# Optimization experiments

Measured on AMD Instinct MI355X. Metric: run time of the kernel, lower is better.

Reference implementation:

```python
import jax, jax.numpy as jnp
import numpy as np

N_NODES = 100000

def setup_inputs() -> dict:
    key = jax.random.key(0)
    k1, k2, k3, k4 = jax.random.split(key, 4)
    B, S, D, H = 50000, 10, 128, 128
    nodes = jax.random.randint(k1, (B,), 0, N_NODES, dtype=jnp.int64 if jax.config.jax_enable_x64 else jnp.int32)
    neigh_idx = jax.random.randint(k2, (B, S), 0, N_NODES, dtype=nodes.dtype)
    feature = jax.random.normal(k3, (N_NODES, D), dtype=jnp.float32)
    weight = jax.random.normal(k4, (2 * D, H), dtype=jnp.float32) * (1.0 / np.sqrt(2 * D))
    return {"nodes": nodes, "neigh_idx": neigh_idx, "feature": feature, "weight": weight}

def reference(nodes, neigh_idx, feature, weight):
    # Mean aggregation over sampled neighbors: [B, S, D] -> [B, D]
    neigh_feats = jnp.mean(feature[neigh_idx], axis=1)
    # Self features: [B, D]
    self_feats = feature[nodes]
    # Concat + linear + ReLU (gcn=False branch)
    combined = jnp.concatenate([self_feats, neigh_feats], axis=1)  # [B, 2D]
    return jax.nn.relu(combined @ weight)  # [B, H]
```

## Files before the change

### kernel.cpp

```cpp
#include <hip/hip_runtime.h>


typedef __attribute__((ext_vector_type(8))) short bf16x8;
typedef __attribute__((ext_vector_type(4))) float f32x4;

#define THREADS 512
#define B_TILE 64

__device__ __forceinline__ unsigned short f2bf(float x) {
  unsigned int u = __float_as_uint(x);
  u += 0x7fffu + ((u >> 16) & 1u);
  return (unsigned short)(u >> 16);
}

__global__ __launch_bounds__(THREADS, 1)
void sage_fused(const int* __restrict__ nodes,
                const int* __restrict__ neigh,
                const float* __restrict__ feat,
                const float* __restrict__ W,
                float* __restrict__ out,
                int B)
{
  constexpr int D = 128, K = 256, H = 128, S = 10;
  constexpr int STR = K + 8;

  __shared__ unsigned short Clds[B_TILE * STR];
  __shared__ unsigned short Wt[H * STR];

  const int t = threadIdx.x;
  const int block0 = blockIdx.x * B_TILE;

  {
    const float4* W4 = (const float4*)W;
#pragma unroll
    for (int i = 0; i < (K * H / 4) / THREADS; ++i) {
      int f4i = i * THREADS + t;
      float4 v = W4[f4i];
      int flat = f4i << 2;
      int k = flat >> 7;
      int h = flat & (H - 1);
      Wt[(h + 0) * STR + k] = f2bf(v.x);
      Wt[(h + 1) * STR + k] = f2bf(v.y);
      Wt[(h + 2) * STR + k] = f2bf(v.z);
      Wt[(h + 3) * STR + k] = f2bf(v.w);
    }
  }

  {
    const int r   = t >> 3;
    const int sub = t & 7;
    const int b   = block0 + r;
    ushort4* cself = (ushort4*)&Clds[r * STR];
    ushort4* cmean = (ushort4*)&Clds[r * STR + D];
    if (b < B) {
      const float4* fbase = (const float4*)feat;
      const long srow = (long)nodes[b] * (D / 4);
      float4 sf[4];
#pragma unroll
      for (int j = 0; j < 4; ++j) sf[j] = fbase[srow + j * 8 + sub];
      float ax[4], ay[4], az[4], aw[4];
#pragma unroll
      for (int j = 0; j < 4; ++j) { ax[j] = 0.f; ay[j] = 0.f; az[j] = 0.f; aw[j] = 0.f; }
#pragma unroll
      for (int s = 0; s < S; ++s) {
        const long nrow = (long)neigh[b * S + s] * (D / 4);
#pragma unroll
        for (int j = 0; j < 4; ++j) {
          float4 v = fbase[nrow + j * 8 + sub];
          ax[j] += v.x; ay[j] += v.y; az[j] += v.z; aw[j] += v.w;
        }
      }
#pragma unroll
      for (int j = 0; j < 4; ++j) {
        int q = j * 8 + sub;
        ushort4 sv, mv;
        sv.x = f2bf(sf[j].x); sv.y = f2bf(sf[j].y);
        sv.z = f2bf(sf[j].z); sv.w = f2bf(sf[j].w);
        mv.x = f2bf(ax[j] * 0.1f); mv.y = f2bf(ay[j] * 0.1f);
        mv.z = f2bf(az[j] * 0.1f); mv.w = f2bf(aw[j] * 0.1f);
        cself[q] = sv;
        cmean[q] = mv;
      }
    } else {
      ushort4 z; z.x = z.y = z.z = z.w = 0;
#pragma unroll
      for (int j = 0; j < 4; ++j) {
        int q = j * 8 + sub;
        cself[q] = z;
        cmean[q] = z;
      }
    }
  }
  __syncthreads();

  const int lane = t & 63;
  const int wave = t >> 6;
  const int m    = lane & 15;
  const int quad = lane >> 4;
  const int rbase = (wave & 1) * 32;
  const int cbase = (wave >> 1) * 32;

  f32x4 acc00 = {0.f, 0.f, 0.f, 0.f};
  f32x4 acc01 = {0.f, 0.f, 0.f, 0.f};
  f32x4 acc10 = {0.f, 0.f, 0.f, 0.f};
  f32x4 acc11 = {0.f, 0.f, 0.f, 0.f};

#pragma unroll
  for (int ks = 0; ks < K / 32; ++ks) {
    const int koff = ks * 32 + quad * 8;
    bf16x8 a0 = *(const bf16x8*)&Clds[(rbase      + m) * STR + koff];
    bf16x8 a1 = *(const bf16x8*)&Clds[(rbase + 16 + m) * STR + koff];
    bf16x8 b0 = *(const bf16x8*)&Wt[(cbase      + m) * STR + koff];
    bf16x8 b1 = *(const bf16x8*)&Wt[(cbase + 16 + m) * STR + koff];
    acc00 = __builtin_amdgcn_mfma_f32_16x16x32_bf16(a0, b0, acc00, 0, 0, 0);
    acc01 = __builtin_amdgcn_mfma_f32_16x16x32_bf16(a0, b1, acc01, 0, 0, 0);
    acc10 = __builtin_amdgcn_mfma_f32_16x16x32_bf16(a1, b0, acc10, 0, 0, 0);
    acc11 = __builtin_amdgcn_mfma_f32_16x16x32_bf16(a1, b1, acc11, 0, 0, 0);
  }

#pragma unroll
  for (int reg = 0; reg < 4; ++reg) {
    const int row0 = rbase + quad * 4 + reg;
    const int row1 = rbase + 16 + quad * 4 + reg;
    const int gb0 = block0 + row0;
    const int gb1 = block0 + row1;
    if (gb0 < B) {
      out[(size_t)gb0 * H + cbase      + m] = fmaxf(acc00[reg], 0.0f);
      out[(size_t)gb0 * H + cbase + 16 + m] = fmaxf(acc01[reg], 0.0f);
    }
    if (gb1 < B) {
      out[(size_t)gb1 * H + cbase      + m] = fmaxf(acc10[reg], 0.0f);
      out[(size_t)gb1 * H + cbase + 16 + m] = fmaxf(acc11[reg], 0.0f);
    }
  }
}

extern "C" void kernel_launch(void* const* d_in, const int* in_sizes, int n_in,
                              void* d_out, int out_size, void* d_ws, size_t ws_size,
                              hipStream_t stream) {
  const int*   nodes = (const int*)d_in[0];
  const int*   neigh = (const int*)d_in[1];
  const float* feat  = (const float*)d_in[2];
  const float* W     = (const float*)d_in[3];
  float*       out   = (float*)d_out;
  const int B = in_sizes[0];
  const int grid = (B + B_TILE - 1) / B_TILE;
  sage_fused<<<grid, THREADS, 0, stream>>>(nodes, neigh, feat, W, out, B);
}
```

Baseline: 149.7 us.

## Split fused SAGE kernel into weight-prep, gather and GEMM kernels

Replaces the single fused kernel with three launches. The first converts W once into a transposed bf16 buffer in the workspace. The second does a high-occupancy neighbor gather that writes bf16 combined rows to the workspace. The third is a GEMM that keeps each wave's W fragments in registers and stages only the activation tile in LDS. The goal is to remove the per-block reconversion of W and the low occupancy of the gather phase, which the old launch bounds and large LDS footprint imposed. In exchange it adds a round trip of the combined matrix through global memory and two extra kernel launches, and it falls back to using the output buffer as scratch if the workspace is too small.

```diff
diff --git a/kernel.cpp b/kernel.cpp
--- a/kernel.cpp
+++ b/kernel.cpp
@@ -3,9 +3,6 @@
 
 typedef __attribute__((ext_vector_type(8))) short bf16x8;
 typedef __attribute__((ext_vector_type(4))) float f32x4;
-
-#define THREADS 512
-#define B_TILE 64
 
 __device__ __forceinline__ unsigned short f2bf(float x) {
   unsigned int u = __float_as_uint(x);
@@ -13,83 +10,85 @@
   return (unsigned short)(u >> 16);
 }
 
-__global__ __launch_bounds__(THREADS, 1)
-void sage_fused(const int* __restrict__ nodes,
-                const int* __restrict__ neigh,
-                const float* __restrict__ feat,
-                const float* __restrict__ W,
-                float* __restrict__ out,
-                int B)
+__global__ void sage_prep_wt(const float* __restrict__ W,
+                             unsigned short* __restrict__ Wt) {
+  int tid = blockIdx.x * blockDim.x + threadIdx.x;
+  const float4* W4 = (const float4*)W;
+  float4 v = W4[tid];
+  int flat = tid << 2;
+  int k = flat >> 7;
+  int h = flat & 127;
+  Wt[(h + 0) * 256 + k] = f2bf(v.x);
+  Wt[(h + 1) * 256 + k] = f2bf(v.y);
+  Wt[(h + 2) * 256 + k] = f2bf(v.z);
+  Wt[(h + 3) * 256 + k] = f2bf(v.w);
+}
+
+__global__ __launch_bounds__(256, 6)
+void sage_gather(const int* __restrict__ nodes,
+                 const int* __restrict__ neigh,
+                 const float* __restrict__ feat,
+                 unsigned short* __restrict__ comb,
+                 int B)
 {
-  constexpr int D = 128, K = 256, H = 128, S = 10;
-  constexpr int STR = K + 8;
+  const int t   = threadIdx.x;
+  const int r   = t >> 4;
+  const int sub = t & 15;
+  const int b   = blockIdx.x * 16 + r;
+  if (b >= B) return;
 
-  __shared__ unsigned short Clds[B_TILE * STR];
-  __shared__ unsigned short Wt[H * STR];
+  const float4* fbase = (const float4*)feat;
+  const long srow = (long)nodes[b] * 32;
+  float4 s0 = fbase[srow + sub];
+  float4 s1 = fbase[srow + 16 + sub];
+
+  float m0x=0.f,m0y=0.f,m0z=0.f,m0w=0.f, m1x=0.f,m1y=0.f,m1z=0.f,m1w=0.f;
+#pragma unroll
+  for (int s = 0; s < 10; ++s) {
+    const long nrow = (long)neigh[b * 10 + s] * 32;
+    float4 v0 = fbase[nrow + sub];
+    float4 v1 = fbase[nrow + 16 + sub];
+    m0x += v0.x; m0y += v0.y; m0z += v0.z; m0w += v0.w;
+    m1x += v1.x; m1y += v1.y; m1z += v1.z; m1w += v1.w;
+  }
+
+  ushort4* crow = (ushort4*)(comb + (size_t)b * 256);
+  ushort4 a, c;
+  a.x = f2bf(s0.x); a.y = f2bf(s0.y); a.z = f2bf(s0.z); a.w = f2bf(s0.w);
+  crow[sub] = a;
+  a.x = f2bf(s1.x); a.y = f2bf(s1.y); a.z = f2bf(s1.z); a.w = f2bf(s1.w);
+  crow[16 + sub] = a;
+  c.x = f2bf(m0x * 0.1f); c.y = f2bf(m0y * 0.1f);
+  c.z = f2bf(m0z * 0.1f); c.w = f2bf(m0w * 0.1f);
+  crow[32 + sub] = c;
+  c.x = f2bf(m1x * 0.1f); c.y = f2bf(m1y * 0.1f);
+  c.z = f2bf(m1z * 0.1f); c.w = f2bf(m1w * 0.1f);
+  crow[48 + sub] = c;
+}
+
+__global__ __launch_bounds__(512, 4)
+void sage_gemm(const unsigned short* __restrict__ comb,
+               const unsigned short* __restrict__ Wt,
+               float* __restrict__ out,
+               int B)
+{
+  constexpr int K = 256, H = 128, STR = K + 8;
+  __shared__ unsigned short Clds[64 * STR];
 
   const int t = threadIdx.x;
-  const int block0 = blockIdx.x * B_TILE;
+  const int block0 = blockIdx.x * 64;
 
-  {
-    const float4* W4 = (const float4*)W;
+  const uint4* c4 = (const uint4*)comb;
 #pragma unroll
-    for (int i = 0; i < (K * H / 4) / THREADS; ++i) {
-      int f4i = i * THREADS + t;
-      float4 v = W4[f4i];
-      int flat = f4i << 2;
-      int k = flat >> 7;
-      int h = flat & (H - 1);
-      Wt[(h + 0) * STR + k] = f2bf(v.x);
-      Wt[(h + 1) * STR + k] = f2bf(v.y);
-      Wt[(h + 2) * STR + k] = f2bf(v.z);
-      Wt[(h + 3) * STR + k] = f2bf(v.w);
-    }
-  }
-
-  {
-    const int r   = t >> 3;
-    const int sub = t & 7;
-    const int b   = block0 + r;
-    ushort4* cself = (ushort4*)&Clds[r * STR];
-    ushort4* cmean = (ushort4*)&Clds[r * STR + D];
-    if (b < B) {
-      const float4* fbase = (const float4*)feat;
-      const long srow = (long)nodes[b] * (D / 4);
-      float4 sf[4];
-#pragma unroll
-      for (int j = 0; j < 4; ++j) sf[j] = fbase[srow + j * 8 + sub];
-      float ax[4], ay[4], az[4], aw[4];
-#pragma unroll
-      for (int j = 0; j < 4; ++j) { ax[j] = 0.f; ay[j] = 0.f; az[j] = 0.f; aw[j] = 0.f; }
-#pragma unroll
-      for (int s = 0; s < S; ++s) {
-        const long nrow = (long)neigh[b * S + s] * (D / 4);
-#pragma unroll
-        for (int j = 0; j < 4; ++j) {
-          float4 v = fbase[nrow + j * 8 + sub];
-          ax[j] += v.x; ay[j] += v.y; az[j] += v.z; aw[j] += v.w;
-        }
-      }
-#pragma unroll
-      for (int j = 0; j < 4; ++j) {
-        int q = j * 8 + sub;
-        ushort4 sv, mv;
-        sv.x = f2bf(sf[j].x); sv.y = f2bf(sf[j].y);
-        sv.z = f2bf(sf[j].z); sv.w = f2bf(sf[j].w);
-        mv.x = f2bf(ax[j] * 0.1f); mv.y = f2bf(ay[j] * 0.1f);
-        mv.z = f2bf(az[j] * 0.1f); mv.w = f2bf(aw[j] * 0.1f);
-        cself[q] = sv;
-        cmean[q] = mv;
-      }
-    } else {
-      ushort4 z; z.x = z.y = z.z = z.w = 0;
-#pragma unroll
-      for (int j = 0; j < 4; ++j) {
-        int q = j * 8 + sub;
-        cself[q] = z;
-        cmean[q] = z;
-      }
-    }
+  for (int p = 0; p < 4; ++p) {
+    int c = p * 512 + t;
+    int row = c >> 5;
+    int off = (c & 31) * 8;
+    int gb = block0 + row;
+    uint4 v;
+    if (gb < B) v = c4[(size_t)gb * 32 + (c & 31)];
+    else { v.x = v.y = v.z = v.w = 0u; }
+    *(uint4*)&Clds[row * STR + off] = v;
   }
   __syncthreads();
 
@@ -97,40 +96,34 @@
   const int wave = t >> 6;
   const int m    = lane & 15;
   const int quad = lane >> 4;
-  const int rbase = (wave & 1) * 32;
-  const int cbase = (wave >> 1) * 32;
+  const int cbase = wave * 16;
 
-  f32x4 acc00 = {0.f, 0.f, 0.f, 0.f};
-  f32x4 acc01 = {0.f, 0.f, 0.f, 0.f};
-  f32x4 acc10 = {0.f, 0.f, 0.f, 0.f};
-  f32x4 acc11 = {0.f, 0.f, 0.f, 0.f};
+  bf16x8 bfrag[8];
+#pragma unroll
+  for (int ks = 0; ks < 8; ++ks)
+    bfrag[ks] = *(const bf16x8*)&Wt[(cbase + m) * K + ks * 32 + quad * 8];
+
+  f32x4 acc[4];
+#pragma unroll
+  for (int rt = 0; rt < 4; ++rt) acc[rt] = (f32x4){0.f, 0.f, 0.f, 0.f};
 
 #pragma unroll
-  for (int ks = 0; ks < K / 32; ++ks) {
+  for (int ks = 0; ks < 8; ++ks) {
     const int koff = ks * 32 + quad * 8;
-    bf16x8 a0 = *(const bf16x8*)&Clds[(rbase      + m) * STR + koff];
-    bf16x8 a1 = *(const bf16x8*)&Clds[(rbase + 16 + m) * STR + koff];
-    bf16x8 b0 = *(const bf16x8*)&Wt[(cbase      + m) * STR + koff];
-    bf16x8 b1 = *(const bf16x8*)&Wt[(cbase + 16 + m) * STR + koff];
-    acc00 = __builtin_amdgcn_mfma_f32_16x16x32_bf16(a0, b0, acc00, 0, 0, 0);
-    acc01 = __builtin_amdgcn_mfma_f32_16x16x32_bf16(a0, b1, acc01, 0, 0, 0);
-    acc10 = __builtin_amdgcn_mfma_f32_16x16x32_bf16(a1, b0, acc10, 0, 0, 0);
-    acc11 = __builtin_amdgcn_mfma_f32_16x16x32_bf16(a1, b1, acc11, 0, 0, 0);
+#pragma unroll
+    for (int rt = 0; rt < 4; ++rt) {
+      bf16x8 a = *(const bf16x8*)&Clds[(rt * 16 + m) * STR + koff];
+      acc[rt] = __builtin_amdgcn_mfma_f32_16x16x32_bf16(a, bfrag[ks], acc[rt], 0, 0, 0);
+    }
   }
 
 #pragma unroll
-  for (int reg = 0; reg < 4; ++reg) {
-    const int row0 = rbase + quad * 4 + reg;
-    const int row1 = rbase + 16 + quad * 4 + reg;
-    const int gb0 = block0 + row0;
-    const int gb1 = block0 + row1;
-    if (gb0 < B) {
-      out[(size_t)gb0 * H + cbase      + m] = fmaxf(acc00[reg], 0.0f);
-      out[(size_t)gb0 * H + cbase + 16 + m] = fmaxf(acc01[reg], 0.0f);
-    }
-    if (gb1 < B) {
-      out[(size_t)gb1 * H + cbase      + m] = fmaxf(acc10[reg], 0.0f);
-      out[(size_t)gb1 * H + cbase + 16 + m] = fmaxf(acc11[reg], 0.0f);
+  for (int rt = 0; rt < 4; ++rt) {
+#pragma unroll
+    for (int reg = 0; reg < 4; ++reg) {
+      const int row = rt * 16 + quad * 4 + reg;
+      const int gb = block0 + row;
+      if (gb < B) out[(size_t)gb * H + cbase + m] = fmaxf(acc[rt][reg], 0.0f);
     }
   }
 }
@@ -144,6 +137,14 @@
   const float* W     = (const float*)d_in[3];
   float*       out   = (float*)d_out;
   const int B = in_sizes[0];
-  const int grid = (B + B_TILE - 1) / B_TILE;
-  sage_fused<<<grid, THREADS, 0, stream>>>(nodes, neigh, feat, W, out, B);
+
+  unsigned short* Wt = (unsigned short*)d_ws;
+  const size_t need = 65536 + (size_t)B * 256 * 2;
+  unsigned short* comb = (ws_size >= need)
+                           ? (unsigned short*)((char*)d_ws + 65536)
+                           : (unsigned short*)d_out;
+
+  sage_prep_wt<<<32, 256, 0, stream>>>(W, Wt);
+  sage_gather<<<(B + 15) / 16, 256, 0, stream>>>(nodes, neigh, feat, comb, B);
+  sage_gemm<<<(B + 63) / 64, 512, 0, stream>>>(comb, Wt, out, B);
 }
```

New measurement: 142.1 us. 1.05x faster.
